# Kernel tuning notes

Hardware: AMD Instinct MI355X
Metric: run time of the kernel (lower is better)

Reference implementation:

```python
import jax, jax.numpy as jnp
import numpy as np

B, LQ, LA, H = 32, 1024, 1024, 512
NEG = -1e7


def setup_inputs() -> dict:
    key = jax.random.key(0)
    kq, ka, ku = jax.random.split(key, 3)
    q = jax.random.normal(kq, (B, LQ, H), dtype=jnp.float32)
    a = jax.random.normal(ka, (B, LA, H), dtype=jnp.float32)
    U = 0.02 * jax.random.normal(ku, (H, H), dtype=jnp.float32)  # init.normal(std=0.02)
    q_mask = jnp.ones((B, LQ, 1), dtype=jnp.float32)
    a_mask = jnp.ones((B, LA, 1), dtype=jnp.float32)
    return {"q": q, "a": a, "U": U, "q_mask": q_mask, "a_mask": a_mask}


def reference(q, a, U, q_mask, a_mask):
    # mask[b,i,j] = q_mask[b,i] * a_mask[b,j]  (nonzero => valid)
    mask = jnp.matmul(q_mask, jnp.swapaxes(a_mask, 1, 2)) > 0  # [B,LQ,LA] bool
    # bilinear score X = q @ U @ a^T
    qU = jnp.einsum('bqh,hk->bqk', q, U)
    X = jnp.einsum('bqk,bak->bqa', qU, a)  # [B,LQ,LA]
    X = jnp.where(mask, X, NEG)
    I = jax.nn.sigmoid(X)
    att_a2q = jnp.max(jax.nn.softmax(I, axis=-1), axis=-1)  # [B,LQ]
    att_q2a = jnp.max(jax.nn.softmax(I, axis=-2), axis=-2)  # [B,LA]
    q_attn = jnp.einsum('blh,bl->bh', q, att_a2q)  # [B,H]
    a_attn = jnp.einsum('blh,bl->bh', a, att_q2a)  # [B,H]
    return q_attn, a_attn
```

## Files before the change

### kernel.cpp

```cpp
#include <hip/hip_runtime.h>

typedef __attribute__((ext_vector_type(8))) short bf16x8;
typedef __attribute__((ext_vector_type(4))) float f32x4;
typedef unsigned short u16;
typedef unsigned int u32;

#define NLOG2E -1.44269504088896f
#define LOG2E   1.44269504088896f
#define SLICE 32768

__device__ __forceinline__ float bf2f(u16 x) {
  union { u32 u; float f; } v; v.u = ((u32)x) << 16; return v.f;
}
__device__ __forceinline__ u16 f2b(float f) {
  union { float f; u32 u; } v; v.f = f;
  return (u16)((v.u + 0x7FFFu + ((v.u >> 16) & 1u)) >> 16);
}
__device__ __forceinline__ u32 pk2(float lo, float hi) {
  return (u32)f2b(lo) | ((u32)f2b(hi) << 16);
}
__device__ __forceinline__ bool inputs_are_bf16(const void* qmask) {
  return *(const u32*)qmask == 0x3F803F80u;
}

__device__ __forceinline__ void convert16(const void* __restrict__ src,
                                          u16* __restrict__ dst, int idx) {
  const float4* s = (const float4*)src + (size_t)idx * 4;
  float4 v0 = s[0], v1 = s[1], v2 = s[2], v3 = s[3];
  uint4* d = (uint4*)dst + (size_t)idx * 2;
  uint4 w0, w1;
  w0.x = pk2(v0.x, v0.y); w0.y = pk2(v0.z, v0.w);
  w0.z = pk2(v1.x, v1.y); w0.w = pk2(v1.z, v1.w);
  w1.x = pk2(v2.x, v2.y); w1.y = pk2(v2.z, v2.w);
  w1.z = pk2(v3.x, v3.y); w1.w = pk2(v3.z, v3.w);
  d[0] = w0;
  d[1] = w1;
}

__global__ __launch_bounds__(256) void prep_all(
    const void* __restrict__ q, const void* __restrict__ a,
    const void* __restrict__ U, const void* __restrict__ qmask,
    u16* __restrict__ qb, u16* __restrict__ ab, u16* __restrict__ Ut,
    float* __restrict__ out)
{
  const bool bf = inputs_are_bf16(qmask);
  const int t = threadIdx.x;
  if (blockIdx.x < 64) {
    const int bb = blockIdx.x;
    out[bb * 512 + t] = 0.f;
    out[bb * 512 + 256 + t] = 0.f;
    __shared__ u16 tile[64][65];
    const int bx = bb & 7, by = bb >> 3;
    #pragma unroll
    for (int i = 0; i < 16; i++) {
      int r = i * 4 + (t >> 6);
      int c = t & 63;
      size_t gi = (size_t)(by * 64 + r) * 512 + bx * 64 + c;
      tile[c][r] = bf ? ((const u16*)U)[gi] : f2b(((const float*)U)[gi]);
    }
    __syncthreads();
    #pragma unroll
    for (int i = 0; i < 16; i++) {
      int r = i * 4 + (t >> 6);
      int c = t & 63;
      Ut[(size_t)(bx * 64 + r) * 512 + by * 64 + c] = tile[r][c];
    }
  } else {
    if (bf) return;
    const int idx = (blockIdx.x - 64) * 256 + t;
    convert16(q, qb, idx);
  }
}

template<int EPI>
__global__ __launch_bounds__(256, 3) void gemm_bt(
    const u16* __restrict__ A, const u16* __restrict__ B,
    u16* __restrict__ C, float scaleC,
    size_t strideA, size_t strideB,
    const void* __restrict__ q_mask, const void* __restrict__ a_mask,
    float* __restrict__ statsP,
    const u16* __restrict__ A_alias, const u16* __restrict__ B_alias,
    const void* __restrict__ conv_src, u16* __restrict__ conv_dst)
{
  const bool bfin = inputs_are_bf16(q_mask);

  if (EPI == 0 && blockIdx.y >= 256) {
    if (bfin) return;
    const int cid = (blockIdx.y - 256) * 4 + blockIdx.x;
    const int idx = cid * 256 + (int)threadIdx.x;
    convert16(conv_src, conv_dst, idx);
    return;
  }

  __shared__ __align__(16) char smem[50176];
  u16* Ct  = (u16*)smem;
  float* redS = (float*)smem;
  float* redM = (float*)(smem + 16896);
  float* colS = (float*)(smem + 33792);
  float* colM = (float*)(smem + 34816);
  float* qp = (float*)(smem + 49152);
  float* ap = (float*)(smem + 49664);

  int bx = blockIdx.x, by = blockIdx.y;
  const int bz = blockIdx.z;
  if (EPI) {
    const int k = blockIdx.x, s = blockIdx.y;
    bx = (k & 3) * 2 + (s & 1);
    by = (k >> 2) * 4 + (s >> 1);
  }
  const int tid  = threadIdx.x;
  const int lane = tid & 63;
  const int wave = tid >> 6;
  const int wr = wave >> 1, wc = wave & 1;
  const int l15 = lane & 15, lq = lane >> 4;

  const u16* Asel = (bfin && A_alias) ? A_alias : A;
  const u16* Bsel = (bfin && B_alias) ? B_alias : B;

  const int srl  = lane >> 2;
  const int sc   = (lane & 3) ^ ((lane >> 3) & 3);
  const size_t sgo = (size_t)srl * 512 + sc * 8;
  const int foff = ((lq ^ ((l15 >> 1) & 3)) * 8);

  const u16* Ab = Asel + strideA * bz + (size_t)by * 128 * 512;
  const u16* Bb = Bsel + strideB * bz + (size_t)bx * 128 * 512;

  if (EPI) {
    if (tid < 128) {
      int gi = bz * 1024 + by * 128 + tid;
      float v = bfin ? bf2f(((const u16*)q_mask)[gi]) : ((const float*)q_mask)[gi];
      qp[tid] = (v > 0.f) ? 0.f : 1e30f;
    } else {
      int gj = bz * 1024 + bx * 128 + (tid - 128);
      float v = bfin ? bf2f(((const u16*)a_mask)[gj]) : ((const float*)a_mask)[gj];
      ap[tid - 128] = (v > 0.f) ? 0.f : 1e30f;
    }
    __syncthreads();
  }

  f32x4 acc[4][4];
  if (EPI) {
    #pragma unroll
    for (int mt = 0; mt < 4; mt++)
      #pragma unroll
      for (int nt = 0; nt < 4; nt++) {
        float cp = ap[wc * 64 + nt * 16 + l15];
        #pragma unroll
        for (int r = 0; r < 4; r++)
          acc[mt][nt][r] = qp[wr * 64 + mt * 16 + lq * 4 + r] + cp;
      }
  } else {
    #pragma unroll
    for (int i = 0; i < 4; i++)
      #pragma unroll
      for (int j = 0; j < 4; j++) {
        f32x4 z = {0.f, 0.f, 0.f, 0.f};
        acc[i][j] = z;
      }
  }

  auto stage32 = [&](int buf, int k0) {
    char* base = smem + buf * 16384;
    #pragma unroll
    for (int i = 0; i < 2; i++) {
      const size_t go = (size_t)(wave * 32 + i * 16) * 512 + k0 + sgo;
      __builtin_amdgcn_global_load_lds(
          (const __attribute__((address_space(1))) void*)(Ab + go),
          (__attribute__((address_space(3))) void*)(base + wave * 2048 + i * 1024), 16, 0, 0);
      __builtin_amdgcn_global_load_lds(
          (const __attribute__((address_space(1))) void*)(Bb + go),
          (__attribute__((address_space(3))) void*)(base + 8192 + wave * 2048 + i * 1024), 16, 0, 0);
    }
  };

  stage32(0, 0);
  stage32(1, 32);
  #pragma unroll
  for (int t = 0; t < 16; t++) {
    if (t + 2 < 16) stage32((t + 2) % 3, (t + 2) * 32);
    if (t <= 13)      asm volatile("s_waitcnt vmcnt(8)\n\ts_barrier" ::: "memory");
    else if (t == 14) asm volatile("s_waitcnt vmcnt(4)\n\ts_barrier" ::: "memory");
    else              asm volatile("s_waitcnt vmcnt(0)\n\ts_barrier" ::: "memory");

    const u16* As = (const u16*)(smem + (t % 3) * 16384);
    const u16* Bs = (const u16*)(smem + (t % 3) * 16384 + 8192);
    bf16x8 af[4], bfr[4];
    #pragma unroll
    for (int tt = 0; tt < 4; tt++) {
      const int ar = wr * 64 + tt * 16 + l15;
      const int br = wc * 64 + tt * 16 + l15;
      af[tt]  = *(const bf16x8*)&As[ar * 32 + foff];
      bfr[tt] = *(const bf16x8*)&Bs[br * 32 + foff];
    }
    #pragma unroll
    for (int mt = 0; mt < 4; mt++)
      #pragma unroll
      for (int nt = 0; nt < 4; nt++)
        acc[mt][nt] = __builtin_amdgcn_mfma_f32_16x16x32_bf16(af[mt], bfr[nt], acc[mt][nt], 0, 0, 0);
    asm volatile("s_waitcnt lgkmcnt(0)\n\ts_barrier" ::: "memory");
  }

  if (!EPI) {
    #pragma unroll
    for (int mt = 0; mt < 4; mt++)
      #pragma unroll
      for (int nt = 0; nt < 4; nt++)
        #pragma unroll
        for (int r = 0; r < 4; r++) {
          int row = wr * 64 + mt * 16 + lq * 4 + r;
          int col = wc * 64 + nt * 16 + l15;
          Ct[row * 144 + col] = f2b(scaleC * acc[mt][nt][r]);
        }
    __syncthreads();
    u16* Cb = C + (size_t)by * 128 * 512 + bx * 128;
    #pragma unroll
    for (int i = 0; i < 8; i++) {
      int c = tid + i * 256;
      int row = c >> 4, cc = c & 15;
      *(bf16x8*)&Cb[(size_t)row * 512 + cc * 8] = *(const bf16x8*)&Ct[row * 144 + cc * 8];
    }
  } else {
    const int gi0 = bz * 1024 + by * 128;
    const int gj0 = bz * 1024 + bx * 128;
    float* rowsumP = statsP + 0      + bx * SLICE;
    float* colsumP = statsP + 262144 + by * SLICE;
    float* rowminP = statsP + 524288 + bx * SLICE;
    float* colminP = statsP + 786432 + by * SLICE;

    float csum[4] = {0.f, 0.f, 0.f, 0.f};
    float cmin[4] = {3e38f, 3e38f, 3e38f, 3e38f};
    #pragma unroll
    for (int mt = 0; mt < 4; mt++) {
      #pragma unroll
      for (int r = 0; r < 4; r++) {
        const int row = wr * 64 + mt * 16 + lq * 4 + r;
        float rsm = 0.f, rmn = 3e38f;
        #pragma unroll
        for (int nt = 0; nt < 4; nt++) {
          float y = acc[mt][nt][r];
          float u = __builtin_amdgcn_exp2f(y);
          float s = __builtin_amdgcn_rcpf(1.f + u);
          float e = __builtin_amdgcn_exp2f(LOG2E * s);
          rsm += e;
          csum[nt] += e;
          rmn = fminf(rmn, y);
          cmin[nt] = fminf(cmin[nt], y);
        }
        redS[row * 33 + l15 + 16 * wc] = rsm;
        redM[row * 33 + l15 + 16 * wc] = rmn;
      }
    }
    #pragma unroll
    for (int nt = 0; nt < 4; nt++) {
      float cs = csum[nt], cm = cmin[nt];
      cs += __shfl_xor(cs, 16); cm = fminf(cm, __shfl_xor(cm, 16));
      cs += __shfl_xor(cs, 32); cm = fminf(cm, __shfl_xor(cm, 32));
      if (lane < 16) {
        int j = wc * 64 + nt * 16 + l15;
        colS[j * 2 + wr] = cs;
        colM[j * 2 + wr] = cm;
      }
    }
    __syncthreads();
    if (tid < 128) {
      float s = 0.f;
      #pragma unroll
      for (int j = 0; j < 32; j++) s += redS[tid * 33 + j];
      rowsumP[gi0 + tid] = s;
      colsumP[gj0 + tid] = colS[tid * 2] + colS[tid * 2 + 1];
    } else {
      const int r = tid - 128;
      float m = 3e38f;
      #pragma unroll
      for (int j = 0; j < 32; j++) m = fminf(m, redM[r * 33 + j]);
      rowminP[gi0 + r] = m;
      colminP[gj0 + r] = fminf(colM[r * 2], colM[r * 2 + 1]);
    }
  }
}

__global__ __launch_bounds__(256) void partial_kernel(
    const u16* __restrict__ qb, const u16* __restrict__ ab,
    const void* __restrict__ q0, const void* __restrict__ a0,
    const void* __restrict__ qmask,
    const float* __restrict__ statsP, float* __restrict__ out)
{
  __shared__ float att[128];
  __shared__ float red[4][512];
  const int tid = threadIdx.x;
  const int seg = blockIdx.x;
  const int b = blockIdx.y >> 1, half = blockIdx.y & 1;
  if (tid < 128) {
    const int g = b * 1024 + seg * 128 + tid;
    const float* sumP = statsP + half * 262144;
    const float* minP = statsP + 524288 + half * 262144;
    float s = 0.f, m = 3e38f;
    #pragma unroll
    for (int s8 = 0; s8 < 8; s8++) {
      s += sumP[s8 * SLICE + g];
      m = fminf(m, minP[s8 * SLICE + g]);
    }
    float Imax = __builtin_amdgcn_rcpf(1.f + __builtin_amdgcn_exp2f(m));
    att[tid] = __expf(Imax) * __builtin_amdgcn_rcpf(s);
  }
  __syncthreads();
  const bool bf = inputs_are_bf16(qmask);
  const u16* base = bf ? (const u16*)(half ? a0 : q0) : (half ? ab : qb);
  const uint4* src = (const uint4*)(base + (size_t)b * 524288
                                    + (size_t)seg * 128 * 512);
  const int rw = tid >> 6;
  const int lane = tid & 63;
  float a0v = 0.f, a1v = 0.f, a2v = 0.f, a3v = 0.f;
  float a4v = 0.f, a5v = 0.f, a6v = 0.f, a7v = 0.f;
  #pragma unroll 8
  for (int i = 0; i < 32; i++) {
    const int row = i * 4 + rw;
    uint4 w = src[(size_t)row * 64 + lane];
    float wt = att[row];
    a0v = fmaf(__uint_as_float(w.x << 16), wt, a0v);
    a1v = fmaf(__uint_as_float(w.x & 0xFFFF0000u), wt, a1v);
    a2v = fmaf(__uint_as_float(w.y << 16), wt, a2v);
    a3v = fmaf(__uint_as_float(w.y & 0xFFFF0000u), wt, a3v);
    a4v = fmaf(__uint_as_float(w.z << 16), wt, a4v);
    a5v = fmaf(__uint_as_float(w.z & 0xFFFF0000u), wt, a5v);
    a6v = fmaf(__uint_as_float(w.w << 16), wt, a6v);
    a7v = fmaf(__uint_as_float(w.w & 0xFFFF0000u), wt, a7v);
  }
  *(float4*)&red[rw][lane * 8]     = make_float4(a0v, a1v, a2v, a3v);
  *(float4*)&red[rw][lane * 8 + 4] = make_float4(a4v, a5v, a6v, a7v);
  __syncthreads();
  const int h = tid * 2;
  float s0 = red[0][h]     + red[1][h]     + red[2][h]     + red[3][h];
  float s1 = red[0][h + 1] + red[1][h + 1] + red[2][h + 1] + red[3][h + 1];
  float* ob = out + half * 16384 + b * 512 + h;
  atomicAdd(&ob[0], s0);
  atomicAdd(&ob[1], s1);
}

extern "C" void kernel_launch(void* const* d_in, const int* in_sizes, int n_in,
                              void* d_out, int out_size, void* d_ws, size_t ws_size,
                              hipStream_t stream) {
  const void* q  = d_in[0];
  const void* a  = d_in[1];
  const void* U  = d_in[2];
  const void* qm = d_in[3];
  const void* am = d_in[4];
  float* out = (float*)d_out;

  char* ws = (char*)d_ws;
  u16* qb    = (u16*)ws;
  u16* ab    = (u16*)(ws + 33554432);
  u16* qU    = (u16*)(ws + 67108864);
  u16* Ut    = (u16*)(ws + 100663296);
  float* statsP = (float*)(ws + 100663296);

  const bool host_bf = (in_sizes[0] == 33554432);
  const int prep_blocks = host_bf ? 64 : 4160;
  const int g0_ny       = host_bf ? 256 : 1280;
  prep_all<<<dim3(prep_blocks), dim3(256), 0, stream>>>(q, a, U, qm, qb, ab, Ut, out);
  gemm_bt<0><<<dim3(4, g0_ny, 1), dim3(256), 0, stream>>>(
      qb, Ut, qU, NLOG2E, (size_t)0, (size_t)0, qm, am, statsP,
      (const u16*)q, (const u16*)nullptr, a, ab);
  gemm_bt<1><<<dim3(8, 8, 32), dim3(256), 0, stream>>>(
      qU, ab, (u16*)nullptr, 1.f, (size_t)524288, (size_t)524288, qm, am, statsP,
      (const u16*)nullptr, (const u16*)a, nullptr, nullptr);
  partial_kernel<<<dim3(8, 64), dim3(256), 0, stream>>>(qb, ab, q, a, qm, statsP, out);
}
```

Baseline: 236.1 us.

## Fuse fp32-to-bf16 conversion of q into qU GEMM A-operand staging

The first GEMM now reads q directly in fp32 through registers, converts it to bf16 and writes it into LDS, so the GEMM no longer waits for a separate q conversion in prep. The q and a bf16 conversions (still needed by later kernels) move into extra blocks of the first GEMM launch instead of the prep kernel, which now only transposes U. This removes a dependency and shortens the prep kernel, at the cost of register-staged A loads with extra VGPR pressure and a larger grid for the first GEMM.

```diff
diff --git a/kernel.cpp b/kernel.cpp
--- a/kernel.cpp
+++ b/kernel.cpp
@@ -45,34 +45,28 @@
 {
   const bool bf = inputs_are_bf16(qmask);
   const int t = threadIdx.x;
-  if (blockIdx.x < 64) {
-    const int bb = blockIdx.x;
-    out[bb * 512 + t] = 0.f;
-    out[bb * 512 + 256 + t] = 0.f;
-    __shared__ u16 tile[64][65];
-    const int bx = bb & 7, by = bb >> 3;
-    #pragma unroll
-    for (int i = 0; i < 16; i++) {
-      int r = i * 4 + (t >> 6);
-      int c = t & 63;
-      size_t gi = (size_t)(by * 64 + r) * 512 + bx * 64 + c;
-      tile[c][r] = bf ? ((const u16*)U)[gi] : f2b(((const float*)U)[gi]);
-    }
-    __syncthreads();
-    #pragma unroll
-    for (int i = 0; i < 16; i++) {
-      int r = i * 4 + (t >> 6);
-      int c = t & 63;
-      Ut[(size_t)(bx * 64 + r) * 512 + by * 64 + c] = tile[r][c];
-    }
-  } else {
-    if (bf) return;
-    const int idx = (blockIdx.x - 64) * 256 + t;
-    convert16(q, qb, idx);
-  }
-}
-
-template<int EPI>
+  const int bb = blockIdx.x;
+  out[bb * 512 + t] = 0.f;
+  out[bb * 512 + 256 + t] = 0.f;
+  __shared__ u16 tile[64][65];
+  const int bx = bb & 7, by = bb >> 3;
+  #pragma unroll
+  for (int i = 0; i < 16; i++) {
+    int r = i * 4 + (t >> 6);
+    int c = t & 63;
+    size_t gi = (size_t)(by * 64 + r) * 512 + bx * 64 + c;
+    tile[c][r] = bf ? ((const u16*)U)[gi] : f2b(((const float*)U)[gi]);
+  }
+  __syncthreads();
+  #pragma unroll
+  for (int i = 0; i < 16; i++) {
+    int r = i * 4 + (t >> 6);
+    int c = t & 63;
+    Ut[(size_t)(bx * 64 + r) * 512 + by * 64 + c] = tile[r][c];
+  }
+}
+
+template<int EPI, int AFP32>
 __global__ __launch_bounds__(256, 3) void gemm_bt(
     const u16* __restrict__ A, const u16* __restrict__ B,
     u16* __restrict__ C, float scaleC,
@@ -80,16 +74,18 @@
     const void* __restrict__ q_mask, const void* __restrict__ a_mask,
     float* __restrict__ statsP,
     const u16* __restrict__ A_alias, const u16* __restrict__ B_alias,
-    const void* __restrict__ conv_src, u16* __restrict__ conv_dst)
+    const void* __restrict__ convQ_src, u16* __restrict__ convQ_dst,
+    const void* __restrict__ convA_src, u16* __restrict__ convA_dst,
+    const float* __restrict__ Af32)
 {
-  const bool bfin = inputs_are_bf16(q_mask);
-
-  if (EPI == 0 && blockIdx.y >= 256) {
-    if (bfin) return;
-    const int cid = (blockIdx.y - 256) * 4 + blockIdx.x;
-    const int idx = cid * 256 + (int)threadIdx.x;
-    convert16(conv_src, conv_dst, idx);
-    return;
+  if constexpr (EPI == 0 && AFP32 == 1) {
+    if (blockIdx.y >= 256) {
+      const int cid = (blockIdx.y - 256) * 4 + blockIdx.x;
+      const int idx = (cid & 4095) * 256 + (int)threadIdx.x;
+      if (cid < 4096) convert16(convQ_src, convQ_dst, idx);
+      else            convert16(convA_src, convA_dst, idx);
+      return;
+    }
   }
 
   __shared__ __align__(16) char smem[50176];
@@ -114,6 +110,7 @@
   const int wr = wave >> 1, wc = wave & 1;
   const int l15 = lane & 15, lq = lane >> 4;
 
+  const bool bfin = inputs_are_bf16(q_mask);
   const u16* Asel = (bfin && A_alias) ? A_alias : A;
   const u16* Bsel = (bfin && B_alias) ? B_alias : B;
 
@@ -159,31 +156,20 @@
       }
   }
 
-  auto stage32 = [&](int buf, int k0) {
-    char* base = smem + buf * 16384;
+  auto stageB = [&](int buf, int k0) {
+    char* base = smem + buf * 16384 + 8192;
     #pragma unroll
     for (int i = 0; i < 2; i++) {
       const size_t go = (size_t)(wave * 32 + i * 16) * 512 + k0 + sgo;
       __builtin_amdgcn_global_load_lds(
-          (const __attribute__((address_space(1))) void*)(Ab + go),
+          (const __attribute__((address_space(1))) void*)(Bb + go),
           (__attribute__((address_space(3))) void*)(base + wave * 2048 + i * 1024), 16, 0, 0);
-      __builtin_amdgcn_global_load_lds(
-          (const __attribute__((address_space(1))) void*)(Bb + go),
-          (__attribute__((address_space(3))) void*)(base + 8192 + wave * 2048 + i * 1024), 16, 0, 0);
     }
   };
 
-  stage32(0, 0);
-  stage32(1, 32);
-  #pragma unroll
-  for (int t = 0; t < 16; t++) {
-    if (t + 2 < 16) stage32((t + 2) % 3, (t + 2) * 32);
-    if (t <= 13)      asm volatile("s_waitcnt vmcnt(8)\n\ts_barrier" ::: "memory");
-    else if (t == 14) asm volatile("s_waitcnt vmcnt(4)\n\ts_barrier" ::: "memory");
-    else              asm volatile("s_waitcnt vmcnt(0)\n\ts_barrier" ::: "memory");
-
+  auto compute = [&](int t) {
     const u16* As = (const u16*)(smem + (t % 3) * 16384);
-    const u16* Bs = (const u16*)(smem + (t % 3) * 16384 + 8192);
+    const u16* Bs = As + 4096;
     bf16x8 af[4], bfr[4];
     #pragma unroll
     for (int tt = 0; tt < 4; tt++) {
@@ -197,7 +183,71 @@
       #pragma unroll
       for (int nt = 0; nt < 4; nt++)
         acc[mt][nt] = __builtin_amdgcn_mfma_f32_16x16x32_bf16(af[mt], bfr[nt], acc[mt][nt], 0, 0, 0);
-    asm volatile("s_waitcnt lgkmcnt(0)\n\ts_barrier" ::: "memory");
+  };
+
+  if constexpr (AFP32) {
+    const float* Ap = Af32 + (size_t)by * 128 * 512
+                    + (size_t)(wave * 32 + srl) * 512 + sc * 8;
+    float4 rs[3][4];
+    auto issueStage = [&](int st) {
+      const int buf = st % 3, k0 = st * 32;
+      stageB(buf, k0);
+      const float* p = Ap + k0;
+      rs[st % 3][0] = *(const float4*)p;
+      rs[st % 3][1] = *(const float4*)(p + 4);
+      rs[st % 3][2] = *(const float4*)(p + 8192);
+      rs[st % 3][3] = *(const float4*)(p + 8196);
+    };
+    auto writeA = [&](int t) {
+      const int s = t % 3;
+      uint4* dst = (uint4*)(smem + (t % 3) * 16384 + wave * 2048 + lane * 16);
+      uint4 w;
+      w.x = pk2(rs[s][0].x, rs[s][0].y); w.y = pk2(rs[s][0].z, rs[s][0].w);
+      w.z = pk2(rs[s][1].x, rs[s][1].y); w.w = pk2(rs[s][1].z, rs[s][1].w);
+      dst[0]  = w;
+      w.x = pk2(rs[s][2].x, rs[s][2].y); w.y = pk2(rs[s][2].z, rs[s][2].w);
+      w.z = pk2(rs[s][3].x, rs[s][3].y); w.w = pk2(rs[s][3].z, rs[s][3].w);
+      dst[64] = w;
+    };
+
+    issueStage(0);
+    issueStage(1);
+    #pragma unroll
+    for (int t = 0; t < 16; t++) {
+      if (t + 2 < 16) issueStage(t + 2);
+      if (t <= 13)      asm volatile("s_waitcnt vmcnt(12)" ::: "memory");
+      else if (t == 14) asm volatile("s_waitcnt vmcnt(6)" ::: "memory");
+      else              asm volatile("s_waitcnt vmcnt(0)" ::: "memory");
+      writeA(t);
+      asm volatile("s_waitcnt lgkmcnt(0)\n\ts_barrier" ::: "memory");
+      compute(t);
+      asm volatile("s_waitcnt lgkmcnt(0)\n\ts_barrier" ::: "memory");
+    }
+  } else {
+    auto stage32 = [&](int buf, int k0) {
+      char* base = smem + buf * 16384;
+      #pragma unroll
+      for (int i = 0; i < 2; i++) {
+        const size_t go = (size_t)(wave * 32 + i * 16) * 512 + k0 + sgo;
+        __builtin_amdgcn_global_load_lds(
+            (const __attribute__((address_space(1))) void*)(Ab + go),
+            (__attribute__((address_space(3))) void*)(base + wave * 2048 + i * 1024), 16, 0, 0);
+        __builtin_amdgcn_global_load_lds(
+            (const __attribute__((address_space(1))) void*)(Bb + go),
+            (__attribute__((address_space(3))) void*)(base + 8192 + wave * 2048 + i * 1024), 16, 0, 0);
+      }
+    };
+    stage32(0, 0);
+    stage32(1, 32);
+    #pragma unroll
+    for (int t = 0; t < 16; t++) {
+      if (t + 2 < 16) stage32((t + 2) % 3, (t + 2) * 32);
+      if (t <= 13)      asm volatile("s_waitcnt vmcnt(8)\n\ts_barrier" ::: "memory");
+      else if (t == 14) asm volatile("s_waitcnt vmcnt(4)\n\ts_barrier" ::: "memory");
+      else              asm volatile("s_waitcnt vmcnt(0)\n\ts_barrier" ::: "memory");
+      compute(t);
+      asm volatile("s_waitcnt lgkmcnt(0)\n\ts_barrier" ::: "memory");
+    }
   }
 
   if (!EPI) {
@@ -355,14 +405,21 @@
   float* statsP = (float*)(ws + 100663296);
 
   const bool host_bf = (in_sizes[0] == 33554432);
-  const int prep_blocks = host_bf ? 64 : 4160;
-  const int g0_ny       = host_bf ? 256 : 1280;
-  prep_all<<<dim3(prep_blocks), dim3(256), 0, stream>>>(q, a, U, qm, qb, ab, Ut, out);
-  gemm_bt<0><<<dim3(4, g0_ny, 1), dim3(256), 0, stream>>>(
-      qb, Ut, qU, NLOG2E, (size_t)0, (size_t)0, qm, am, statsP,
-      (const u16*)q, (const u16*)nullptr, a, ab);
-  gemm_bt<1><<<dim3(8, 8, 32), dim3(256), 0, stream>>>(
+  prep_all<<<dim3(64), dim3(256), 0, stream>>>(q, a, U, qm, qb, ab, Ut, out);
+  if (host_bf) {
+    gemm_bt<0, 0><<<dim3(4, 256, 1), dim3(256), 0, stream>>>(
+        qb, Ut, qU, NLOG2E, (size_t)0, (size_t)0, qm, am, statsP,
+        (const u16*)q, (const u16*)nullptr,
+        nullptr, nullptr, nullptr, nullptr, nullptr);
+  } else {
+    gemm_bt<0, 1><<<dim3(4, 2304, 1), dim3(256), 0, stream>>>(
+        qb, Ut, qU, NLOG2E, (size_t)0, (size_t)0, qm, am, statsP,
+        (const u16*)nullptr, (const u16*)nullptr,
+        q, qb, a, ab, (const float*)q);
+  }
+  gemm_bt<1, 0><<<dim3(8, 8, 32), dim3(256), 0, stream>>>(
       qU, ab, (u16*)nullptr, 1.f, (size_t)524288, (size_t)524288, qm, am, statsP,
-      (const u16*)nullptr, (const u16*)a, nullptr, nullptr);
+      (const u16*)nullptr, (const u16*)a,
+      nullptr, nullptr, nullptr, nullptr, nullptr);
   partial_kernel<<<dim3(8, 64), dim3(256), 0, stream>>>(qb, ab, q, a, qm, statsP, out);
 }
```

Measured after the change: 272.4 us. 1.15x slower.
